# Optimization experiments

Measured on AMD Instinct MI355X. Metric: run time of the kernel, lower is better.

Reference implementation:

```python
import jax, jax.numpy as jnp
import numpy as np

# GemNet sizes
N_EDGES = 80_000
N_TRIP = 640_000      # intermediate triplets (cbf rows)
N_QUAD = 1_280_000    # quadruplets
KMAX = 24             # max quadruplets per edge (padded)
NUM_SPH = 7
E_EDGE, E_QUAD, E_BIL, E_RBF, E_CBF, E_SBF = 128, 64, 64, 16, 16, 32

INV_SQRT_2 = 1.0 / np.sqrt(2.0)
SILU_SCALE = 1.0 / 0.6  # GemNet ScaledSiLU


def scaled_silu(x):
    return jax.nn.silu(x) * SILU_SCALE


def setup_inputs() -> dict:
    key = jax.random.key(0)
    ks = jax.random.split(key, 16)
    s = 0.05
    inp = {
        'm': jax.random.normal(ks[0], (N_EDGES, E_EDGE), jnp.float32),
        'rbf': jax.random.normal(ks[1], (N_EDGES, E_RBF), jnp.float32),
        'cbf': jax.random.normal(ks[2], (N_TRIP, E_CBF), jnp.float32),
        'sbf_W1': jax.random.normal(ks[3], (N_EDGES, E_SBF, NUM_SPH), jnp.float32) * s,
        'sbf_sph': jax.random.normal(ks[4], (N_EDGES, KMAX, NUM_SPH), jnp.float32) * s,
        # consistent ragged indexing: quadruplet q maps to edge q%N_EDGES at slot q//N_EDGES (< KMAX)
        'Kidx4': jnp.arange(N_QUAD, dtype=jnp.int32) // N_EDGES,
        'id4_reduce_ca': jnp.arange(N_QUAD, dtype=jnp.int32) % N_EDGES,
        'id_swap': jnp.arange(N_EDGES, dtype=jnp.int32).reshape(-1, 2)[:, ::-1].reshape(-1),
        'id4_expand_intm_db': jax.random.randint(ks[5], (N_TRIP,), 0, N_EDGES, jnp.int32),
        'id4_expand_abd': jax.random.randint(ks[6], (N_QUAD,), 0, N_TRIP, jnp.int32),
        # parameters (Dense layers are bias-free)
        'W_dense_db': jax.random.normal(ks[7], (E_EDGE, E_EDGE), jnp.float32) * s,
        'W_rbf': jax.random.normal(ks[8], (E_RBF, E_EDGE), jnp.float32) * s,
        'W_cbf': jax.random.normal(ks[9], (E_CBF, E_QUAD), jnp.float32) * s,
        'W_down': jax.random.normal(ks[10], (E_EDGE, E_QUAD), jnp.float32) * s,
        'W_bil': jax.random.normal(ks[11], (E_QUAD, E_SBF, E_BIL), jnp.float32) * s,
        'W_up_ca': jax.random.normal(ks[12], (E_BIL, E_EDGE), jnp.float32) * s,
        'W_up_ac': jax.random.normal(ks[13], (E_BIL, E_EDGE), jnp.float32) * s,
    }
    return inp


def reference(m, rbf, cbf, sbf_W1, sbf_sph,
              W_dense_db, W_rbf, W_cbf, W_down, W_bil, W_up_ca, W_up_ac,
              Kidx4, id_swap, id4_reduce_ca, id4_expand_intm_db, id4_expand_abd):
    # dense_db + Hadamard with projected rbf (ScalingFactor scale == 1.0 with scale_file=None)
    x_db = scaled_silu(m @ W_dense_db)           # (nEdges, E_EDGE)
    x_db = x_db * (rbf @ W_rbf)                  # scale_rbf (scale=1)
    x_db = scaled_silu(x_db @ W_down)            # (nEdges, E_QUAD)
    x_db = x_db[id4_expand_intm_db]              # (nTrip, E_QUAD)
    x_db = x_db * (cbf @ W_cbf)                  # scale_cbf (scale=1)
    x_db = x_db[id4_expand_abd]                  # (nQuad, E_QUAD)

    # EfficientInteractionBilinear: scatter quadruplets into (nEdges, Kmax, E_QUAD)
    n_edges, kmax = sbf_sph.shape[0], sbf_sph.shape[1]
    m2 = jnp.zeros((n_edges, kmax, x_db.shape[1]), x_db.dtype)
    m2 = m2.at[id4_reduce_ca, Kidx4].set(x_db)
    sum_k = jnp.einsum('eks,ekc->esc', sbf_sph, m2)    # (nEdges, NUM_SPH, E_QUAD)
    t = jnp.einsum('eis,esc->eic', sbf_W1, sum_k)      # (nEdges, E_SBF, E_QUAD)
    x = jnp.einsum('eic,cio->eo', t, W_bil)            # (nEdges, E_BIL); scale_sbf_sum (scale=1)

    x_ca = scaled_silu(x @ W_up_ca)              # (nEdges, E_EDGE)
    x_ac = scaled_silu(x @ W_up_ac)[id_swap]
    return (x_ca + x_ac) * INV_SQRT_2
```

## Files before the change

### kernel.cpp

```cpp
#include <hip/hip_runtime.h>
#include <hip/hip_bf16.h>

#define NEDGES 80000
#define NTRIP  640000
#define NQUAD  1280000

typedef __attribute__((ext_vector_type(8))) short short8;
typedef __attribute__((ext_vector_type(4))) float f32x4;

__device__ __forceinline__ unsigned short f2bf(float f) {
  __hip_bfloat16 h = __float2bfloat16(f);
  return reinterpret_cast<unsigned short&>(h);
}
__device__ __forceinline__ float bf2f(short s) {
  union { unsigned u; float f; } u;
  u.u = ((unsigned)(unsigned short)s) << 16;
  return u.f;
}
__device__ __forceinline__ float sSiLU(float x) {
  return x * (1.0f / 0.6f) / (1.0f + __expf(-x));
}

__device__ __forceinline__ void pack_one(const float* __restrict__ W,
                                         unsigned short* __restrict__ dst,
                                         int p, int NT, int Ksrc, int N) {
  int j = p & 7;
  int l = (p >> 3) & 63;
  int rest = p >> 9;
  int nt = rest % NT;
  int kb = rest / NT;
  int k = kb * 32 + ((l >> 4) << 3) + j;
  int n = nt * 16 + (l & 15);
  float v = (k < Ksrc) ? W[(size_t)k * N + n] : 0.0f;
  dst[p] = f2bf(v);
}

__global__ __launch_bounds__(256) void kpack(
    const float* __restrict__ Wd, const float* __restrict__ Wrbf,
    const float* __restrict__ Wdown, const float* __restrict__ Wbil,
    const float* __restrict__ Wupca, const float* __restrict__ Wupac,
    unsigned short* __restrict__ WdP, unsigned short* __restrict__ WrbfP,
    unsigned short* __restrict__ WdownP, unsigned short* __restrict__ WbilP,
    unsigned short* __restrict__ WupcaP, unsigned short* __restrict__ WupacP) {
  int idx = blockIdx.x * 256 + threadIdx.x;
  if (idx < 16384)        pack_one(Wd,    WdP,    idx,          8, 128,  128);
  else if (idx < 20480)   pack_one(Wrbf,  WrbfP,  idx - 16384,  8, 16,   128);
  else if (idx < 28672)   pack_one(Wdown, WdownP, idx - 20480,  4, 128,  64);
  else if (idx < 159744)  pack_one(Wbil,  WbilP,  idx - 28672,  4, 2048, 64);
  else if (idx < 167936)  pack_one(Wupca, WupcaP, idx - 159744, 8, 64,   128);
  else if (idx < 176128)  pack_one(Wupac, WupacP, idx - 167936, 8, 64,   128);
}

__global__ __launch_bounds__(256) void kA(
    const float* __restrict__ m, const float* __restrict__ rbf,
    const unsigned short* __restrict__ WdP, const unsigned short* __restrict__ WrbfP,
    const unsigned short* __restrict__ WdownP, unsigned short* __restrict__ x_down) {
  __shared__ unsigned short h_lds[4][16][136];
  const int tid = threadIdx.x;
  const int w = tid >> 6, l = tid & 63;
  const int el = l & 15, g = l >> 4;
  const int ebase = blockIdx.x * 64 + w * 16;

  short8 am[4];
  {
    const float* mrow = m + (size_t)(ebase + el) * 128 + g * 8;
#pragma unroll
    for (int kb = 0; kb < 4; ++kb) {
      const f32x4 lo = *reinterpret_cast<const f32x4*>(mrow + kb * 32);
      const f32x4 hi = *reinterpret_cast<const f32x4*>(mrow + kb * 32 + 4);
      short8 a;
      a[0] = f2bf(lo[0]); a[1] = f2bf(lo[1]); a[2] = f2bf(lo[2]); a[3] = f2bf(lo[3]);
      a[4] = f2bf(hi[0]); a[5] = f2bf(hi[1]); a[6] = f2bf(hi[2]); a[7] = f2bf(hi[3]);
      am[kb] = a;
    }
  }
  short8 ar;
  {
    const float* rrow = rbf + (size_t)(ebase + el) * 16 + (g & 1) * 8;
    const f32x4 lo = *reinterpret_cast<const f32x4*>(rrow);
    const f32x4 hi = *reinterpret_cast<const f32x4*>(rrow + 4);
    ar[0] = f2bf(lo[0]); ar[1] = f2bf(lo[1]); ar[2] = f2bf(lo[2]); ar[3] = f2bf(lo[3]);
    ar[4] = f2bf(hi[0]); ar[5] = f2bf(hi[1]); ar[6] = f2bf(hi[2]); ar[7] = f2bf(hi[3]);
  }

  f32x4 acc1[8], acc2[8];
  const f32x4 z = {0.f, 0.f, 0.f, 0.f};
#pragma unroll
  for (int nt = 0; nt < 8; ++nt) { acc1[nt] = z; acc2[nt] = z; }

#pragma unroll
  for (int kb = 0; kb < 4; ++kb) {
#pragma unroll
    for (int nt = 0; nt < 8; ++nt) {
      short8 b = *reinterpret_cast<const short8*>(WdP + (((kb * 8 + nt) * 64 + l) << 3));
      acc1[nt] = __builtin_amdgcn_mfma_f32_16x16x32_bf16(am[kb], b, acc1[nt], 0, 0, 0);
    }
  }
#pragma unroll
  for (int nt = 0; nt < 8; ++nt) {
    short8 b = *reinterpret_cast<const short8*>(WrbfP + ((nt * 64 + l) << 3));
    acc2[nt] = __builtin_amdgcn_mfma_f32_16x16x32_bf16(ar, b, acc2[nt], 0, 0, 0);
  }

#pragma unroll
  for (int nt = 0; nt < 8; ++nt)
#pragma unroll
    for (int r = 0; r < 4; ++r) {
      float h = sSiLU(acc1[nt][r]) * acc2[nt][r];
      h_lds[w][g * 4 + r][nt * 16 + el] = f2bf(h);
    }
  __syncthreads();

  f32x4 acc3[4];
#pragma unroll
  for (int nt = 0; nt < 4; ++nt) acc3[nt] = z;
#pragma unroll
  for (int kb = 0; kb < 4; ++kb) {
    short8 a = *reinterpret_cast<const short8*>(&h_lds[w][el][kb * 32 + g * 8]);
#pragma unroll
    for (int nt = 0; nt < 4; ++nt) {
      short8 b = *reinterpret_cast<const short8*>(WdownP + (((kb * 4 + nt) * 64 + l) << 3));
      acc3[nt] = __builtin_amdgcn_mfma_f32_16x16x32_bf16(a, b, acc3[nt], 0, 0, 0);
    }
  }
#pragma unroll
  for (int nt = 0; nt < 4; ++nt)
#pragma unroll
    for (int r = 0; r < 4; ++r)
      x_down[(size_t)(ebase + g * 4 + r) * 64 + nt * 16 + el] = f2bf(sSiLU(acc3[nt][r]));
}

__global__ __launch_bounds__(256) void kG(
    const float* __restrict__ cbf, const int* __restrict__ intm,
    const unsigned short* __restrict__ x_down, const float* __restrict__ Wcbf,
    unsigned short* __restrict__ y) {
  __shared__ float cbf_lds[4][16][16];
  const int tid = threadIdx.x;
  const int w = tid >> 6, c = tid & 63;
  const int wid = blockIdx.x * 4 + w;

  float wc[16];
#pragma unroll
  for (int r = 0; r < 16; ++r) wc[r] = Wcbf[r * 64 + c];

#pragma unroll
  for (int it = 0; it < 4; ++it) {
    const int t0 = (wid * 4 + it) * 16;

    const int ivv = intm[t0 + (c & 15)];
    const f32x4 cq = *reinterpret_cast<const f32x4*>(
        cbf + (size_t)(t0 + (c >> 2)) * 16 + (c & 3) * 4);
    *reinterpret_cast<f32x4*>(&cbf_lds[w][c >> 2][(c & 3) * 4]) = cq;

    int es[16];
#pragma unroll
    for (int k = 0; k < 16; ++k) es[k] = __builtin_amdgcn_readlane(ivv, k);

    unsigned short xr[16];
#pragma unroll
    for (int k = 0; k < 16; ++k) xr[k] = x_down[(size_t)es[k] * 64 + c];

#pragma unroll
    for (int j = 0; j < 16; ++j) {
      const f32x4* cr = reinterpret_cast<const f32x4*>(&cbf_lds[w][j][0]);
      const f32x4 q0 = cr[0], q1 = cr[1], q2 = cr[2], q3 = cr[3];
      float proj = 0.f;
#pragma unroll
      for (int r = 0; r < 4; ++r) {
        proj = fmaf(q0[r], wc[r], proj);
        proj = fmaf(q1[r], wc[4 + r], proj);
        proj = fmaf(q2[r], wc[8 + r], proj);
        proj = fmaf(q3[r], wc[12 + r], proj);
      }
      y[(size_t)(t0 + j) * 64 + c] = f2bf(bf2f((short)xr[j]) * proj);
    }
  }
}

__global__ __launch_bounds__(256) void kS2(
    const float* __restrict__ sph, const int* __restrict__ abd,
    const unsigned short* __restrict__ y, unsigned short* __restrict__ sumk) {
  __shared__ float sph_lds[4][172];
  const int tid = threadIdx.x;
  const int w = tid >> 6, c = tid & 63;
  const int wid = blockIdx.x * 4 + w;

#pragma unroll
  for (int it = 0; it < 8; ++it) {
    const int e = wid * 8 + it;

    const int tvv = abd[(size_t)(c & 15) * NEDGES + e];
    if (c < 42)
      *reinterpret_cast<f32x4*>(&sph_lds[w][c * 4]) =
          *reinterpret_cast<const f32x4*>(sph + (size_t)e * 168 + c * 4);

    int te[16];
#pragma unroll
    for (int k = 0; k < 16; ++k) te[k] = __builtin_amdgcn_readlane(tvv, k);

    unsigned short yv[16];
#pragma unroll
    for (int k = 0; k < 16; ++k) yv[k] = y[(size_t)te[k] * 64 + c];

    float sk[7] = {0.f, 0.f, 0.f, 0.f, 0.f, 0.f, 0.f};
#pragma unroll
    for (int k = 0; k < 16; ++k) {
      const float row = bf2f((short)yv[k]);
#pragma unroll
      for (int s = 0; s < 7; ++s) sk[s] = fmaf(sph_lds[w][k * 7 + s], row, sk[s]);
    }
    short8 sv;
#pragma unroll
    for (int s = 0; s < 7; ++s) sv[s] = (short)f2bf(sk[s]);
    sv[7] = 0;
    *reinterpret_cast<short8*>(sumk + (size_t)e * 512 + c * 8) = sv;
  }
}

__global__ __launch_bounds__(256) void kS(
    const float* __restrict__ cbf, const float* __restrict__ sph,
    const int* __restrict__ abd, const int* __restrict__ intm,
    const unsigned short* __restrict__ x_down, const float* __restrict__ Wcbf,
    unsigned short* __restrict__ sumk) {
  __shared__ float cbf_lds[4][16][16];
  __shared__ int   te_lds[4][16];
  __shared__ float sph_lds[4][172];
  const int tid = threadIdx.x;
  const int w = tid >> 6, c = tid & 63;
  const int e = blockIdx.x * 4 + w;

  const int tvv = abd[(size_t)(c & 15) * NEDGES + e];
  if (c < 42)
    *reinterpret_cast<f32x4*>(&sph_lds[w][c * 4]) =
        *reinterpret_cast<const f32x4*>(sph + (size_t)e * 168 + c * 4);
  const int ivv = intm[tvv];
  if (c < 16) te_lds[w][c] = tvv;

  float wc[16];
#pragma unroll
  for (int r = 0; r < 16; ++r) wc[r] = Wcbf[r * 64 + c];

  int es[16];
#pragma unroll
  for (int k = 0; k < 16; ++k) es[k] = __builtin_amdgcn_readlane(ivv, k);

  const int tq = te_lds[w][c >> 2];
  const f32x4 cq = *reinterpret_cast<const f32x4*>(cbf + (size_t)tq * 16 + (c & 3) * 4);

  unsigned short xr[16];
#pragma unroll
  for (int k = 0; k < 16; ++k) xr[k] = x_down[(size_t)es[k] * 64 + c];

  *reinterpret_cast<f32x4*>(&cbf_lds[w][c >> 2][(c & 3) * 4]) = cq;

  float sk[7] = {0.f, 0.f, 0.f, 0.f, 0.f, 0.f, 0.f};
#pragma unroll
  for (int k = 0; k < 16; ++k) {
    const f32x4* cr = reinterpret_cast<const f32x4*>(&cbf_lds[w][k][0]);
    const f32x4 q0 = cr[0], q1 = cr[1], q2 = cr[2], q3 = cr[3];
    float proj = 0.f;
#pragma unroll
    for (int r = 0; r < 4; ++r) {
      proj = fmaf(q0[r], wc[r], proj);
      proj = fmaf(q1[r], wc[4 + r], proj);
      proj = fmaf(q2[r], wc[8 + r], proj);
      proj = fmaf(q3[r], wc[12 + r], proj);
    }
    const float row = bf2f((short)xr[k]) * proj;
#pragma unroll
    for (int s = 0; s < 7; ++s) sk[s] = fmaf(sph_lds[w][k * 7 + s], row, sk[s]);
  }
  short8 sv;
#pragma unroll
  for (int s = 0; s < 7; ++s) sv[s] = (short)f2bf(sk[s]);
  sv[7] = 0;
  *reinterpret_cast<short8*>(sumk + (size_t)e * 512 + c * 8) = sv;
}

__global__ __launch_bounds__(256) void kB2(
    const float* __restrict__ sbfW1, const unsigned short* __restrict__ sumk,
    const unsigned short* __restrict__ WbilP, const unsigned short* __restrict__ WupcaP,
    const unsigned short* __restrict__ WupacP, float* __restrict__ out) {
  __shared__ unsigned short sk_lds[4][16][520];
  __shared__ unsigned short x_lds[4][16][72];
  const int tid = threadIdx.x;
  const int w = tid >> 6, l = tid & 63;
  const int el = l & 15, g = l >> 4;
  const int ebase = blockIdx.x * 64 + w * 16;

#pragma unroll
  for (int i = 0; i < 16; ++i) {
    const short8 v = *reinterpret_cast<const short8*>(sumk + (size_t)(ebase + i) * 512 + l * 8);
    *reinterpret_cast<short8*>(&sk_lds[w][i][l * 8]) = v;
  }

  float w1r[56];
  {
    const f32x4* wp = reinterpret_cast<const f32x4*>(sbfW1 + (size_t)(ebase + el) * 224 + g * 56);
#pragma unroll
    for (int qq = 0; qq < 14; ++qq) {
      f32x4 v = wp[qq];
      w1r[qq * 4 + 0] = v[0]; w1r[qq * 4 + 1] = v[1];
      w1r[qq * 4 + 2] = v[2]; w1r[qq * 4 + 3] = v[3];
    }
  }
  __syncthreads();

  const f32x4 z = {0.f, 0.f, 0.f, 0.f};
  f32x4 acc[4];
#pragma unroll
  for (int nt = 0; nt < 4; ++nt) acc[nt] = z;

#pragma unroll 4
  for (int kb = 0; kb < 64; ++kb) {
    const short8 skv = *reinterpret_cast<const short8*>(&sk_lds[w][el][kb * 8]);
    float skf[7];
#pragma unroll
    for (int s = 0; s < 7; ++s) skf[s] = bf2f(skv[s]);
    short8 a;
#pragma unroll
    for (int j = 0; j < 8; ++j) {
      float t = 0.f;
#pragma unroll
      for (int s = 0; s < 7; ++s) t = fmaf(w1r[j * 7 + s], skf[s], t);
      a[j] = (short)f2bf(t);
    }
    const unsigned short* bp = WbilP + (((kb * 4) * 64 + l) << 3);
#pragma unroll
    for (int nt = 0; nt < 4; ++nt) {
      short8 b = *reinterpret_cast<const short8*>(bp + ((nt * 64) << 3));
      acc[nt] = __builtin_amdgcn_mfma_f32_16x16x32_bf16(a, b, acc[nt], 0, 0, 0);
    }
  }

#pragma unroll
  for (int nt = 0; nt < 4; ++nt)
#pragma unroll
    for (int r = 0; r < 4; ++r)
      x_lds[w][g * 4 + r][nt * 16 + el] = f2bf(acc[nt][r]);
  __syncthreads();

  f32x4 aca[8], acb[8];
#pragma unroll
  for (int nt = 0; nt < 8; ++nt) { aca[nt] = z; acb[nt] = z; }
#pragma unroll
  for (int kb = 0; kb < 2; ++kb) {
    short8 a = *reinterpret_cast<const short8*>(&x_lds[w][el][kb * 32 + g * 8]);
#pragma unroll
    for (int nt = 0; nt < 8; ++nt) {
      short8 b1 = *reinterpret_cast<const short8*>(WupcaP + (((kb * 8 + nt) * 64 + l) << 3));
      short8 b2 = *reinterpret_cast<const short8*>(WupacP + (((kb * 8 + nt) * 64 + l) << 3));
      aca[nt] = __builtin_amdgcn_mfma_f32_16x16x32_bf16(a, b1, aca[nt], 0, 0, 0);
      acb[nt] = __builtin_amdgcn_mfma_f32_16x16x32_bf16(a, b2, acb[nt], 0, 0, 0);
    }
  }
  const float inv = 0.70710678118654752f;
#pragma unroll
  for (int nt = 0; nt < 8; ++nt)
#pragma unroll
    for (int r = 0; r < 4; ++r) {
      float v = (sSiLU(aca[nt][r]) + sSiLU(acb[nt][r ^ 1])) * inv;
      out[(size_t)(ebase + g * 4 + r) * 128 + nt * 16 + el] = v;
    }
}

extern "C" void kernel_launch(void* const* d_in, const int* in_sizes, int n_in,
                              void* d_out, int out_size, void* d_ws, size_t ws_size,
                              hipStream_t stream) {
  const float* m     = (const float*)d_in[0];
  const float* rbf   = (const float*)d_in[1];
  const float* cbf   = (const float*)d_in[2];
  const float* sbfW1 = (const float*)d_in[3];
  const float* sph   = (const float*)d_in[4];
  const int* intm = (const int*)d_in[8];
  const int* abd  = (const int*)d_in[9];
  const float* Wd    = (const float*)d_in[10];
  const float* Wrbf  = (const float*)d_in[11];
  const float* Wcbf  = (const float*)d_in[12];
  const float* Wdown = (const float*)d_in[13];
  const float* Wbil  = (const float*)d_in[14];
  const float* Wupca = (const float*)d_in[15];
  const float* Wupac = (const float*)d_in[16];

  char* ws = (char*)d_ws;
  unsigned short* WdP    = (unsigned short*)(ws + 0);
  unsigned short* WrbfP  = (unsigned short*)(ws + 32768);
  unsigned short* WdownP = (unsigned short*)(ws + 40960);
  unsigned short* WbilP  = (unsigned short*)(ws + 57344);
  unsigned short* WupcaP = (unsigned short*)(ws + 319488);
  unsigned short* WupacP = (unsigned short*)(ws + 335872);
  unsigned short* x_down = (unsigned short*)(ws + 352256);
  unsigned short* y      = (unsigned short*)(ws + 352256 + 10240000);
  unsigned short* sumk2  = (unsigned short*)(ws + 352256 + 10240000 + 81920000);
  unsigned short* sumk1  = y;
  const size_t needed_split = 352256ull + 10240000ull + 81920000ull + 81920000ull;
  const size_t needed_fused = 352256ull + 10240000ull + 81920000ull;

  kpack<<<688, 256, 0, stream>>>(Wd, Wrbf, Wdown, Wbil, Wupca, Wupac,
                                 WdP, WrbfP, WdownP, WbilP, WupcaP, WupacP);
  kA<<<1250, 256, 0, stream>>>(m, rbf, WdP, WrbfP, WdownP, x_down);
  if (ws_size >= needed_split) {
    kG<<<2500, 256, 0, stream>>>(cbf, intm, x_down, Wcbf, y);
    kS2<<<2500, 256, 0, stream>>>(sph, abd, y, sumk2);
    kB2<<<1250, 256, 0, stream>>>(sbfW1, sumk2, WbilP, WupcaP, WupacP, (float*)d_out);
  } else {
    kS<<<20000, 256, 0, stream>>>(cbf, sph, abd, intm, x_down, Wcbf, sumk1);
    kB2<<<1250, 256, 0, stream>>>(sbfW1, sumk1, WbilP, WupcaP, WupacP, (float*)d_out);
  }
}
```

Before: 265.5 us.

## Split bilinear stage across K halves and move up-projection to separate kernel

```diff
diff --git a/kernel.cpp b/kernel.cpp
--- a/kernel.cpp
+++ b/kernel.cpp
@@ -277,7 +277,126 @@
   *reinterpret_cast<short8*>(sumk + (size_t)e * 512 + c * 8) = sv;
 }
 
-__global__ __launch_bounds__(256) void kB2(
+__global__ __launch_bounds__(256) void kB3(
+    const float* __restrict__ sbfW1, const unsigned short* __restrict__ sumk,
+    const unsigned short* __restrict__ WbilP, float* __restrict__ xpart) {
+  __shared__ unsigned short stg[4][2][16][72];
+  const int tid = threadIdx.x;
+  const int w = tid >> 6, l = tid & 63;
+  const int el = l & 15, g = l >> 4;
+  const int gw = blockIdx.x * 4 + w;
+  const int eb = gw >> 1, kh = gw & 1;
+  const int ebase = eb * 16;
+  const int sr = l >> 3, sq = l & 7;
+
+  float w1r[56];
+  {
+    const f32x4* wp = reinterpret_cast<const f32x4*>(sbfW1 + (size_t)(ebase + el) * 224 + g * 56);
+#pragma unroll
+    for (int qq = 0; qq < 14; ++qq) {
+      f32x4 v = wp[qq];
+      w1r[qq * 4 + 0] = v[0]; w1r[qq * 4 + 1] = v[1];
+      w1r[qq * 4 + 2] = v[2]; w1r[qq * 4 + 3] = v[3];
+    }
+  }
+
+  const unsigned short* base = sumk + (size_t)ebase * 512 + kh * 256;
+  short8 ld0 = *reinterpret_cast<const short8*>(base + (size_t)sr * 512 + sq * 8);
+  short8 ld1 = *reinterpret_cast<const short8*>(base + (size_t)(sr + 8) * 512 + sq * 8);
+
+  const f32x4 z = {0.f, 0.f, 0.f, 0.f};
+  f32x4 acc[4];
+#pragma unroll
+  for (int nt = 0; nt < 4; ++nt) acc[nt] = z;
+
+#pragma unroll
+  for (int s = 0; s < 4; ++s) {
+    const int b = s & 1;
+    *reinterpret_cast<short8*>(&stg[w][b][sr][sq * 8]) = ld0;
+    *reinterpret_cast<short8*>(&stg[w][b][sr + 8][sq * 8]) = ld1;
+    if (s < 3) {
+      ld0 = *reinterpret_cast<const short8*>(base + (size_t)sr * 512 + (s + 1) * 64 + sq * 8);
+      ld1 = *reinterpret_cast<const short8*>(base + (size_t)(sr + 8) * 512 + (s + 1) * 64 + sq * 8);
+    }
+#pragma unroll
+    for (int kk = 0; kk < 8; ++kk) {
+      const short8 skv = *reinterpret_cast<const short8*>(&stg[w][b][el][kk * 8]);
+      float skf[7];
+#pragma unroll
+      for (int s7 = 0; s7 < 7; ++s7) skf[s7] = bf2f(skv[s7]);
+      short8 a;
+#pragma unroll
+      for (int j = 0; j < 8; ++j) {
+        float t = 0.f;
+#pragma unroll
+        for (int s7 = 0; s7 < 7; ++s7) t = fmaf(w1r[j * 7 + s7], skf[s7], t);
+        a[j] = (short)f2bf(t);
+      }
+      const int kbg = kh * 32 + s * 8 + kk;
+      const unsigned short* bp = WbilP + (((kbg * 4) * 64 + l) << 3);
+#pragma unroll
+      for (int nt = 0; nt < 4; ++nt) {
+        short8 bb = *reinterpret_cast<const short8*>(bp + ((nt * 64) << 3));
+        acc[nt] = __builtin_amdgcn_mfma_f32_16x16x32_bf16(a, bb, acc[nt], 0, 0, 0);
+      }
+    }
+  }
+
+  float* po = xpart + (size_t)kh * (NEDGES * 64);
+#pragma unroll
+  for (int nt = 0; nt < 4; ++nt)
+#pragma unroll
+    for (int r = 0; r < 4; ++r)
+      po[(size_t)(ebase + g * 4 + r) * 64 + nt * 16 + el] = acc[nt][r];
+}
+
+__global__ __launch_bounds__(256) void kU(
+    const float* __restrict__ xpart, const unsigned short* __restrict__ WupcaP,
+    const unsigned short* __restrict__ WupacP, float* __restrict__ out) {
+  const int tid = threadIdx.x;
+  const int w = tid >> 6, l = tid & 63;
+  const int el = l & 15, g = l >> 4;
+  const int ebase = (blockIdx.x * 4 + w) * 16;
+
+  const float* p0 = xpart + (size_t)(ebase + el) * 64;
+  const float* p1 = p0 + (size_t)NEDGES * 64;
+
+  const f32x4 z = {0.f, 0.f, 0.f, 0.f};
+  f32x4 aca[8], acb[8];
+#pragma unroll
+  for (int nt = 0; nt < 8; ++nt) { aca[nt] = z; acb[nt] = z; }
+
+#pragma unroll
+  for (int kb = 0; kb < 2; ++kb) {
+    const f32x4 a0 = *reinterpret_cast<const f32x4*>(p0 + kb * 32 + g * 8);
+    const f32x4 a1 = *reinterpret_cast<const f32x4*>(p0 + kb * 32 + g * 8 + 4);
+    const f32x4 b0 = *reinterpret_cast<const f32x4*>(p1 + kb * 32 + g * 8);
+    const f32x4 b1 = *reinterpret_cast<const f32x4*>(p1 + kb * 32 + g * 8 + 4);
+    short8 a;
+#pragma unroll
+    for (int j = 0; j < 4; ++j) {
+      a[j]     = (short)f2bf(a0[j] + b0[j]);
+      a[4 + j] = (short)f2bf(a1[j] + b1[j]);
+    }
+#pragma unroll
+    for (int nt = 0; nt < 8; ++nt) {
+      short8 w1 = *reinterpret_cast<const short8*>(WupcaP + (((kb * 8 + nt) * 64 + l) << 3));
+      short8 w2 = *reinterpret_cast<const short8*>(WupacP + (((kb * 8 + nt) * 64 + l) << 3));
+      aca[nt] = __builtin_amdgcn_mfma_f32_16x16x32_bf16(a, w1, aca[nt], 0, 0, 0);
+      acb[nt] = __builtin_amdgcn_mfma_f32_16x16x32_bf16(a, w2, acb[nt], 0, 0, 0);
+    }
+  }
+  const float inv = 0.70710678118654752f;
+#pragma unroll
+  for (int nt = 0; nt < 8; ++nt)
+#pragma unroll
+    for (int r = 0; r < 4; ++r) {
+      float v = (sSiLU(aca[nt][r]) + sSiLU(acb[nt][r ^ 1])) * inv;
+      out[(size_t)(ebase + g * 4 + r) * 128 + nt * 16 + el] = v;
+    }
+}
+
+__global__ __launch_bounds__(256) void kB2f(
     const float* __restrict__ sbfW1, const unsigned short* __restrict__ sumk,
     const unsigned short* __restrict__ WbilP, const unsigned short* __restrict__ WupcaP,
     const unsigned short* __restrict__ WupacP, float* __restrict__ out) {
@@ -391,20 +510,21 @@
   unsigned short* WupacP = (unsigned short*)(ws + 335872);
   unsigned short* x_down = (unsigned short*)(ws + 352256);
   unsigned short* y      = (unsigned short*)(ws + 352256 + 10240000);
-  unsigned short* sumk2  = (unsigned short*)(ws + 352256 + 10240000 + 81920000);
-  unsigned short* sumk1  = y;
+  unsigned short* sumk   = (unsigned short*)(ws + 352256 + 10240000 + 81920000);
+  float*          xpart  = (float*)y;
+  unsigned short* sumk_f = y;
   const size_t needed_split = 352256ull + 10240000ull + 81920000ull + 81920000ull;
-  const size_t needed_fused = 352256ull + 10240000ull + 81920000ull;
 
   kpack<<<688, 256, 0, stream>>>(Wd, Wrbf, Wdown, Wbil, Wupca, Wupac,
                                  WdP, WrbfP, WdownP, WbilP, WupcaP, WupacP);
   kA<<<1250, 256, 0, stream>>>(m, rbf, WdP, WrbfP, WdownP, x_down);
   if (ws_size >= needed_split) {
     kG<<<2500, 256, 0, stream>>>(cbf, intm, x_down, Wcbf, y);
-    kS2<<<2500, 256, 0, stream>>>(sph, abd, y, sumk2);
-    kB2<<<1250, 256, 0, stream>>>(sbfW1, sumk2, WbilP, WupcaP, WupacP, (float*)d_out);
+    kS2<<<2500, 256, 0, stream>>>(sph, abd, y, sumk);
+    kB3<<<2500, 256, 0, stream>>>(sbfW1, sumk, WbilP, xpart);
+    kU<<<1250, 256, 0, stream>>>(xpart, WupcaP, WupacP, (float*)d_out);
   } else {
-    kS<<<20000, 256, 0, stream>>>(cbf, sph, abd, intm, x_down, Wcbf, sumk1);
-    kB2<<<1250, 256, 0, stream>>>(sbfW1, sumk1, WbilP, WupcaP, WupacP, (float*)d_out);
-  }
-}
+    kS<<<20000, 256, 0, stream>>>(cbf, sph, abd, intm, x_down, Wcbf, sumk_f);
+    kB2f<<<1250, 256, 0, stream>>>(sbfW1, sumk_f, WbilP, WupcaP, WupacP, (float*)d_out);
+  }
+}
```

Measured after the change: 292.3 us. +10.1%, slower.
